# Kernel tuning notes

Hardware: AMD Instinct MI355X
Metric: run time of the kernel (lower is better)

Reference implementation:

```python
import jax, jax.numpy as jnp
import numpy as np

N1, N2, N3 = 262144, 65536, 16384
E1, E2 = 524288, 262144
IN_DIM, HID, HEADS, OUT_DIM = 128, 64, 4, 64
NEG_SLOPE = 0.2   # PyG GATConv default negative_slope
BN_EPS = 1e-5


def setup_inputs() -> dict:
    key = jax.random.key(0)
    ks = jax.random.split(key, 13)
    g = lambda k, shape, scale: jax.random.normal(k, shape, jnp.float32) * scale
    HD = HEADS * HID
    return {
        "x": jax.random.normal(ks[0], (N1, IN_DIM), jnp.float32),
        "W1_src": g(ks[1], (IN_DIM, HD), 1.0 / np.sqrt(IN_DIM)),
        "W1_dst": g(ks[2], (IN_DIM, HD), 1.0 / np.sqrt(IN_DIM)),
        "att1_src": g(ks[3], (HEADS, HID), 1.0 / np.sqrt(HID)),
        "att1_dst": g(ks[4], (HEADS, HID), 1.0 / np.sqrt(HID)),
        "b1": jnp.zeros((HD,), jnp.float32),
        "gamma": jnp.ones((HD,), jnp.float32),
        "beta": jnp.zeros((HD,), jnp.float32),
        "run_mean": jnp.zeros((HD,), jnp.float32),
        "run_var": jnp.ones((HD,), jnp.float32),
        "W2_src": g(ks[5], (HD, OUT_DIM), 1.0 / np.sqrt(HD)),
        "W2_dst": g(ks[6], (HD, OUT_DIM), 1.0 / np.sqrt(HD)),
        "att2_src": g(ks[7], (1, OUT_DIM), 1.0 / np.sqrt(OUT_DIM)),
        "att2_dst": g(ks[8], (1, OUT_DIM), 1.0 / np.sqrt(OUT_DIM)),
        "b2": jnp.zeros((OUT_DIM,), jnp.float32),
        "src1": jax.random.randint(ks[9], (E1,), 0, N1),
        "dst1": jax.random.randint(ks[10], (E1,), 0, N2),
        "src2": jax.random.randint(ks[11], (E2,), 0, N2),
        "dst2": jax.random.randint(ks[12], (E2,), 0, N3),
    }


def gat_conv(x_src, x_dst, W_src, W_dst, att_src, att_dst, bias, src, dst, num_dst, heads, ch):
    """PyG GATConv (bipartite, add_self_loops=False, concat)."""
    h_src = (x_src @ W_src).reshape(-1, heads, ch)   # [N, H, C]
    h_dst = (x_dst @ W_dst).reshape(-1, heads, ch)   # [M, H, C]
    a_src = jnp.sum(h_src * att_src, axis=-1)        # [N, H]
    a_dst = jnp.sum(h_dst * att_dst, axis=-1)        # [M, H]
    e = a_src[src] + a_dst[dst]                      # [E, H] gather
    e = jnp.where(e > 0, e, NEG_SLOPE * e)           # leaky_relu
    # segment softmax over destination nodes
    emax = jax.ops.segment_max(e, dst, num_segments=num_dst)
    emax = jax.lax.stop_gradient(jnp.where(jnp.isfinite(emax), emax, 0.0))
    p = jnp.exp(e - emax[dst])
    denom = jax.ops.segment_sum(p, dst, num_segments=num_dst)
    alpha = p / jnp.maximum(denom[dst], 1e-16)       # [E, H]
    msg = alpha[:, :, None] * h_src[src]             # [E, H, C]
    out = jax.ops.segment_sum(msg, dst, num_segments=num_dst)  # scatter-add
    return out.reshape(num_dst, heads * ch) + bias


def reference(x, W1_src, W1_dst, att1_src, att1_dst, b1, gamma, beta, run_mean, run_var,
              W2_src, W2_dst, att2_src, att2_dst, b2, src1, dst1, src2, dst2):
    # layer 1: GATConv((x, x_target), edge_index) with 4 heads, concat
    h = gat_conv(x, x[:N2], W1_src, W1_dst, att1_src, att1_dst, b1,
                 src1, dst1, N2, HEADS, HID)
    # BatchNorm1d in eval mode (running stats), then ELU; dropout is identity in eval
    h = (h - run_mean) * gamma / jnp.sqrt(run_var + BN_EPS) + beta
    h = jax.nn.elu(h)
    # layer 2: GATConv with heads=1
    out = gat_conv(h, h[:N3], W2_src, W2_dst, att2_src, att2_dst, b2,
                   src2, dst2, N3, 1, OUT_DIM)
    return out
```

## Files before the change

### kernel.cpp

```cpp
#include <hip/hip_runtime.h>


constexpr int N1 = 262144, N2 = 65536, N3 = 16384;
constexpr int E1 = 524288, E2 = 262144;
constexpr int IN_DIM = 128, HID = 64, HEADS = 4, OUT_DIM = 64;
constexpr int HD = HEADS * HID;
constexpr float NEG_SLOPE = 0.2f;
constexpr float BN_EPS = 1e-5f;

typedef __attribute__((ext_vector_type(8))) short bf16x8;
typedef __attribute__((ext_vector_type(8))) unsigned short ushort8;
typedef __attribute__((ext_vector_type(4))) float f32x4;

#define GLOAD_LDS16(gp, lp)                                              \
  __builtin_amdgcn_global_load_lds(                                      \
      (const __attribute__((address_space(1))) unsigned int*)(gp),       \
      (__attribute__((address_space(3))) unsigned int*)(lp), 16, 0, 0)

__device__ inline unsigned short f2bf(float f) {
  unsigned u = __float_as_uint(f);
  u += 0x7FFFu + ((u >> 16) & 1u);
  return (unsigned short)(u >> 16);
}

__global__ __launch_bounds__(256) void setup_k(
    const float* __restrict__ W1s, const float* __restrict__ W1d,
    const float* __restrict__ A1s, const float* __restrict__ A1d,
    const float* __restrict__ W2s, const float* __restrict__ W2d,
    const float* __restrict__ A2s, const float* __restrict__ A2d,
    const float* __restrict__ b1, const float* __restrict__ gamma,
    const float* __restrict__ beta, const float* __restrict__ mean,
    const float* __restrict__ var,
    float* __restrict__ wa1s, float* __restrict__ wa1d,
    float* __restrict__ wa2s, float* __restrict__ wa2d,
    float* __restrict__ bnsc, float* __restrict__ bnsh,
    int* __restrict__ deg1, int* __restrict__ deg2,
    int* __restrict__ rp1, int* __restrict__ rp2,
    float* __restrict__ a2s, float* __restrict__ a2d,
    unsigned short* __restrict__ w1T, unsigned short* __restrict__ w2T) {
  int b = blockIdx.x, tid = threadIdx.x;
  if (b < 4) {
    int t = b * 256 + tid;
    if (t < HEADS * IN_DIM) {
      int h = t >> 7, k = t & 127;
      float s = 0.f, d = 0.f;
      for (int c = 0; c < HID; ++c) {
        s += W1s[k * HD + h * HID + c] * A1s[h * HID + c];
        d += W1d[k * HD + h * HID + c] * A1d[h * HID + c];
      }
      wa1s[t] = s; wa1d[t] = d;
    } else if (t < HEADS * IN_DIM + HD) {
      int k = t - HEADS * IN_DIM;
      float s = 0.f, d = 0.f;
      for (int c = 0; c < OUT_DIM; ++c) {
        s += W2s[k * OUT_DIM + c] * A2s[c];
        d += W2d[k * OUT_DIM + c] * A2d[c];
      }
      wa2s[k] = s; wa2d[k] = d;
    } else if (t < HEADS * IN_DIM + 2 * HD) {
      int c = t - HEADS * IN_DIM - HD;
      float sc = gamma[c] * rsqrtf(var[c] + BN_EPS);
      bnsc[c] = sc;
      bnsh[c] = beta[c] + (b1[c] - mean[c]) * sc;
    }
  } else if (b < 68) {
    int i = (b - 4) * 256 + tid;
    int stride = 64 * 256;
    for (int j = i; j < N2; j += stride) { deg1[j] = 0; a2s[j] = 0.f; }
    for (int j = i; j < N3; j += stride) { deg2[j] = 0; a2d[j] = 0.f; }
    if (i == 0) { rp1[0] = 0; rp2[0] = 0; }
  } else if (b < 84) {
    int t = (b - 68) * 256 + tid;
    int n = t >> 4, g = t & 15;
    ushort8 o;
#pragma unroll
    for (int j = 0; j < 8; ++j) o[j] = f2bf(W1s[(size_t)(g * 8 + j) * HD + n]);
    *reinterpret_cast<ushort8*>(w1T + (size_t)n * IN_DIM + (size_t)(g ^ (n & 7)) * 8) = o;
  } else {
    int t = (b - 84) * 256 + tid;
    int n = t >> 5, G = t & 31;
    int k0 = G * 8;
    ushort8 o;
#pragma unroll
    for (int j = 0; j < 8; ++j) o[j] = f2bf(W2s[(size_t)(k0 + j) * OUT_DIM + n]);
    int idx = ((k0 >> 7) << 7) + ((k0 & 127) ^ ((n & 7) << 3));
    *reinterpret_cast<ushort8*>(w2T + (size_t)n * HD + idx) = o;
  }
}

__global__ __launch_bounds__(256) void hist12_k(
    const int* __restrict__ dst1, int* __restrict__ deg1, int* __restrict__ rank1,
    const int* __restrict__ dst2, int* __restrict__ deg2, int* __restrict__ rank2) {
  int b = blockIdx.x;
  if (b < E1 / 256) {
    int i = b * 256 + threadIdx.x;
    rank1[i] = atomicAdd(&deg1[dst1[i]], 1);
  } else {
    int i = (b - E1 / 256) * 256 + threadIdx.x;
    rank2[i] = atomicAdd(&deg2[dst2[i]], 1);
  }
}

__device__ inline void scan_body(const int* in, int* out, int* bsums, int n, int b) {
  __shared__ int s[256];
  int tid = threadIdx.x;
  int i0 = b * 1024 + tid * 4;
  int x0 = in[i0], x1 = in[i0 + 1], x2 = in[i0 + 2], x3 = in[i0 + 3];
  int t = x0 + x1 + x2 + x3;
  s[tid] = t;
  __syncthreads();
  for (int off = 1; off < 256; off <<= 1) {
    int v = (tid >= off) ? s[tid - off] : 0;
    __syncthreads();
    s[tid] += v;
    __syncthreads();
  }
  int base = s[tid] - t;
  out[i0] = base + x0;
  out[i0 + 1] = base + x0 + x1;
  out[i0 + 2] = base + x0 + x1 + x2;
  out[i0 + 3] = base + t;
  if (tid == 255) bsums[b] = s[255];
  (void)n;
}

__global__ __launch_bounds__(256) void scanA_k(
    const int* __restrict__ deg1, int* __restrict__ o1, int* __restrict__ bs1,
    const int* __restrict__ deg2, int* __restrict__ o2, int* __restrict__ bs2) {
  int b = blockIdx.x;
  if (b < 64) scan_body(deg1, o1, bs1, N2, b);
  else scan_body(deg2, o2, bs2, N3, b - 64);
}

__global__ void scanB_k(int* __restrict__ bs1, int* __restrict__ bs2) {
  __shared__ int s[256];
  int* bs = (blockIdx.x == 0) ? bs1 : bs2;
  int nb = (blockIdx.x == 0) ? 64 : 16;
  int tid = threadIdx.x;
  s[tid] = (tid < nb) ? bs[tid] : 0;
  __syncthreads();
  for (int off = 1; off < 256; off <<= 1) {
    int v = (tid >= off) ? s[tid - off] : 0;
    __syncthreads();
    s[tid] += v;
    __syncthreads();
  }
  if (tid < nb) bs[tid] = s[tid];
}

__global__ __launch_bounds__(256) void scanC_k(
    int* __restrict__ o1, const int* __restrict__ bs1,
    int* __restrict__ o2, const int* __restrict__ bs2) {
  int b = blockIdx.x;
  int* out; const int* bs; int bb;
  if (b < 64) { out = o1; bs = bs1; bb = b; }
  else { out = o2; bs = bs2; bb = b - 64; }
  if (bb == 0) return;
  int add = bs[bb - 1];
  int i0 = bb * 1024 + threadIdx.x * 4;
  out[i0] += add; out[i0 + 1] += add; out[i0 + 2] += add; out[i0 + 3] += add;
}

__global__ __launch_bounds__(256) void conv_scores1(
    const float* __restrict__ x, const float* __restrict__ wa_s,
    const float* __restrict__ wa_d, float* __restrict__ a_src,
    float* __restrict__ a_dst) {
  __shared__ float ws[HEADS * IN_DIM], wd[HEADS * IN_DIM];
  int tid = threadIdx.x;
  for (int i = tid; i < HEADS * IN_DIM; i += 256) { ws[i] = wa_s[i]; wd[i] = wa_d[i]; }
  __syncthreads();
  int row = blockIdx.x * 16 + (tid >> 4);
  int g = tid & 15;
  float4 v0 = *reinterpret_cast<const float4*>(x + (size_t)row * IN_DIM + g * 8);
  float4 v1 = *reinterpret_cast<const float4*>(x + (size_t)row * IN_DIM + g * 8 + 4);
  float xv[8] = {v0.x, v0.y, v0.z, v0.w, v1.x, v1.y, v1.z, v1.w};
#pragma unroll
  for (int h = 0; h < HEADS; ++h) {
    float p = 0.f;
#pragma unroll
    for (int j = 0; j < 8; ++j) p = fmaf(xv[j], ws[h * IN_DIM + g * 8 + j], p);
#pragma unroll
    for (int off = 1; off < 16; off <<= 1) p += __shfl_xor(p, off, 64);
    if (g == 0) a_src[(size_t)row * HEADS + h] = p;
  }
  if (row < N2) {
#pragma unroll
    for (int h = 0; h < HEADS; ++h) {
      float p = 0.f;
#pragma unroll
      for (int j = 0; j < 8; ++j) p = fmaf(xv[j], wd[h * IN_DIM + g * 8 + j], p);
#pragma unroll
      for (int off = 1; off < 16; off <<= 1) p += __shfl_xor(p, off, 64);
      if (g == 0) a_dst[(size_t)row * HEADS + h] = p;
    }
  }
}

__global__ __launch_bounds__(256) void scatter1p_k(
    const int* __restrict__ src, const int* __restrict__ dst,
    const int* __restrict__ rp, const int* __restrict__ rank,
    const float* __restrict__ a1s, const float* __restrict__ a1d,
    int* __restrict__ srcs, float4* __restrict__ pexp) {
  int i = blockIdx.x * 256 + threadIdx.x;
  int s = src[i], d = dst[i];
  float4 as = *reinterpret_cast<const float4*>(a1s + (size_t)s * HEADS);
  float4 ad = *reinterpret_cast<const float4*>(a1d + (size_t)d * HEADS);
  float4 p;
#pragma unroll
  for (int h = 0; h < 4; ++h) {
    float e = ((const float*)&as)[h] + ((const float*)&ad)[h];
    e = e > 0.f ? e : NEG_SLOPE * e;
    ((float*)&p)[h] = __expf(e);
  }
  int pos = rp[d] + rank[i];
  srcs[pos] = s;
  pexp[pos] = p;
}

__global__ __launch_bounds__(256) void agg1x(
    const int* __restrict__ rp, const int* __restrict__ srcs,
    const float4* __restrict__ pexp, const float* __restrict__ x,
    unsigned short* __restrict__ z) {
  int d = blockIdx.x * 4 + (threadIdx.x >> 6);
  int lane = threadIdx.x & 63;
  int beg = rp[d], end = rp[d + 1];
  float z0[4] = {0.f, 0.f, 0.f, 0.f}, z1[4] = {0.f, 0.f, 0.f, 0.f};
  float ss[4] = {0.f, 0.f, 0.f, 0.f}, ss2[4] = {0.f, 0.f, 0.f, 0.f};
  int j = beg;
  for (; j + 2 <= end; j += 2) {
    int s0 = srcs[j], s1 = srcs[j + 1];
    float4 p0 = pexp[j], p1 = pexp[j + 1];
    float2 v0 = *reinterpret_cast<const float2*>(x + (size_t)s0 * IN_DIM + lane * 2);
    float2 v1 = *reinterpret_cast<const float2*>(x + (size_t)s1 * IN_DIM + lane * 2);
#pragma unroll
    for (int h = 0; h < 4; ++h) {
      float ph0 = ((const float*)&p0)[h], ph1 = ((const float*)&p1)[h];
      z0[h] = fmaf(ph0, v0.x, fmaf(ph1, v1.x, z0[h]));
      z1[h] = fmaf(ph0, v0.y, fmaf(ph1, v1.y, z1[h]));
      ss[h] += ph0; ss2[h] += ph1;
    }
  }
  if (j < end) {
    int s0 = srcs[j];
    float4 p0 = pexp[j];
    float2 v0 = *reinterpret_cast<const float2*>(x + (size_t)s0 * IN_DIM + lane * 2);
#pragma unroll
    for (int h = 0; h < 4; ++h) {
      float ph0 = ((const float*)&p0)[h];
      z0[h] = fmaf(ph0, v0.x, z0[h]);
      z1[h] = fmaf(ph0, v0.y, z1[h]);
      ss[h] += ph0;
    }
  }
  int G = lane >> 2;
  int idx = ((G ^ (d & 7)) << 3) + ((lane & 3) << 1);
#pragma unroll
  for (int h = 0; h < 4; ++h) {
    float inv = 1.f / fmaxf(ss[h] + ss2[h], 1e-30f);
    unsigned out = (unsigned)f2bf(z0[h] * inv) | ((unsigned)f2bf(z1[h] * inv) << 16);
    *reinterpret_cast<unsigned*>(z + ((size_t)h * N2 + d) * IN_DIM + idx) = out;
  }
}

__global__ __launch_bounds__(256) void finalize1(
    const unsigned short* __restrict__ z, const unsigned short* __restrict__ w1T,
    const float* __restrict__ bnsc, const float* __restrict__ bnsh,
    const float* __restrict__ wa2s, const float* __restrict__ wa2d,
    unsigned short* __restrict__ acc1, float* __restrict__ a2s,
    float* __restrict__ a2d) {
  __shared__ char sm[49152];
  const int tid = threadIdx.x, wave = tid >> 6, lane = tid & 63;
  const int row0 = blockIdx.x * 128;
  const int h = blockIdx.y;
  const char* gA = (const char*)(z + ((size_t)h * N2 + row0) * IN_DIM);
  const char* gB = (const char*)(w1T + (size_t)h * 64 * IN_DIM);
#pragma unroll
  for (int it = 0; it < 8; ++it) {
    int off = it * 4096 + wave * 1024 + lane * 16;
    GLOAD_LDS16(gA + off, sm + off);
  }
#pragma unroll
  for (int it = 0; it < 4; ++it) {
    int off = it * 4096 + wave * 1024 + lane * 16;
    GLOAD_LDS16(gB + off, sm + 32768 + off);
  }
  __syncthreads();
  const int rbase = wave * 32;
  const int kl = (lane >> 4) * 8, fr = lane & 15;
  f32x4 acc[2][4] = {};
#pragma unroll
  for (int ks = 0; ks < 4; ++ks) {
    int k0 = ks * 32 + kl;
    bf16x8 a[2], b[4];
#pragma unroll
    for (int i = 0; i < 2; ++i) {
      int ra = rbase + i * 16 + fr;
      a[i] = *reinterpret_cast<const bf16x8*>(
          sm + ((size_t)ra * 128 + (k0 ^ ((ra & 7) << 3))) * 2);
    }
#pragma unroll
    for (int jj = 0; jj < 4; ++jj) {
      int cb = jj * 16 + fr;
      b[jj] = *reinterpret_cast<const bf16x8*>(
          sm + 32768 + ((size_t)cb * 128 + (k0 ^ ((cb & 7) << 3))) * 2);
    }
#pragma unroll
    for (int i = 0; i < 2; ++i)
#pragma unroll
      for (int jj = 0; jj < 4; ++jj)
        acc[i][jj] = __builtin_amdgcn_mfma_f32_16x16x32_bf16(a[i], b[jj], acc[i][jj], 0, 0, 0);
  }
  float sc[4], sh[4], w2sv[4], w2dv[4];
#pragma unroll
  for (int jj = 0; jj < 4; ++jj) {
    int c = h * 64 + jj * 16 + fr;
    sc[jj] = bnsc[c]; sh[jj] = bnsh[c]; w2sv[jj] = wa2s[c]; w2dv[jj] = wa2d[c];
  }
  const int g = lane >> 4;
#pragma unroll
  for (int i = 0; i < 2; ++i) {
#pragma unroll
    for (int q = 0; q < 4; ++q) {
      int row = row0 + rbase + i * 16 + g * 4 + q;
      float s2s = 0.f, s2d = 0.f;
#pragma unroll
      for (int jj = 0; jj < 4; ++jj) {
        float v = acc[i][jj][q] * sc[jj] + sh[jj];
        v = v > 0.f ? v : expm1f(v);
        s2s = fmaf(v, w2sv[jj], s2s);
        s2d = fmaf(v, w2dv[jj], s2d);
        int c = h * 64 + jj * 16 + fr;
        int idx = ((c >> 7) << 7) + ((c & 127) ^ ((row & 7) << 3));
        acc1[(size_t)row * HD + idx] = f2bf(v);
      }
#pragma unroll
      for (int off = 1; off < 16; off <<= 1) {
        s2s += __shfl_xor(s2s, off, 64);
        s2d += __shfl_xor(s2d, off, 64);
      }
      if (fr == 0) {
        atomicAdd(&a2s[row], s2s);
        if (row < N3) atomicAdd(&a2d[row], s2d);
      }
    }
  }
}

__global__ __launch_bounds__(256) void scatter2p_k(
    const int* __restrict__ src, const int* __restrict__ dst,
    const int* __restrict__ rp, const int* __restrict__ rank,
    const float* __restrict__ a2s, const float* __restrict__ a2d,
    int* __restrict__ srcs, float* __restrict__ pexp) {
  int i = blockIdx.x * 256 + threadIdx.x;
  int s = src[i], d = dst[i];
  float e = a2s[s] + a2d[d];
  e = e > 0.f ? e : NEG_SLOPE * e;
  int pos = rp[d] + rank[i];
  srcs[pos] = s;
  pexp[pos] = __expf(e);
}

__global__ __launch_bounds__(256) void gemm2(
    const unsigned short* __restrict__ acc1, const unsigned short* __restrict__ w2T,
    float* __restrict__ h2) {
  __shared__ char sm[65536];
  const int tid = threadIdx.x, wave = tid >> 6, lane = tid & 63;
  const int row0 = blockIdx.x * 128;
  const char* gB = (const char*)w2T;
#pragma unroll
  for (int it = 0; it < 8; ++it) {
    int off = it * 4096 + wave * 1024 + lane * 16;
    GLOAD_LDS16(gB + off, sm + 32768 + off);
  }
  const int rbase = wave * 32;
  const int kl = (lane >> 4) * 8, fr = lane & 15;
  f32x4 acc[2][4] = {};
  for (int kh = 0; kh < 2; ++kh) {
    __syncthreads();
#pragma unroll
    for (int it = 0; it < 8; ++it) {
      int r = it * 16 + (tid >> 4);
      const char* srcp = (const char*)(acc1 + (size_t)(row0 + r) * HD) +
                         kh * 256 + (tid & 15) * 16;
      GLOAD_LDS16(srcp, sm + it * 4096 + tid * 16);
    }
    __syncthreads();
#pragma unroll
    for (int ks = 0; ks < 4; ++ks) {
      int k0 = ks * 32 + kl;
      bf16x8 a[2], b[4];
#pragma unroll
      for (int i = 0; i < 2; ++i) {
        int ra = rbase + i * 16 + fr;
        a[i] = *reinterpret_cast<const bf16x8*>(
            sm + ((size_t)ra * 128 + (k0 ^ ((ra & 7) << 3))) * 2);
      }
#pragma unroll
      for (int jj = 0; jj < 4; ++jj) {
        int cb = jj * 16 + fr;
        b[jj] = *reinterpret_cast<const bf16x8*>(
            sm + 32768 + ((size_t)cb * 256 + kh * 128 + (k0 ^ ((cb & 7) << 3))) * 2);
      }
#pragma unroll
      for (int i = 0; i < 2; ++i)
#pragma unroll
        for (int jj = 0; jj < 4; ++jj)
          acc[i][jj] = __builtin_amdgcn_mfma_f32_16x16x32_bf16(a[i], b[jj], acc[i][jj], 0, 0, 0);
    }
  }
  const int g = lane >> 4;
#pragma unroll
  for (int i = 0; i < 2; ++i)
#pragma unroll
    for (int q = 0; q < 4; ++q) {
      int row = row0 + rbase + i * 16 + g * 4 + q;
#pragma unroll
      for (int jj = 0; jj < 4; ++jj)
        h2[(size_t)row * OUT_DIM + jj * 16 + fr] = acc[i][jj][q];
    }
}

__global__ __launch_bounds__(256) void agg2(
    const int* __restrict__ rp, const int* __restrict__ srcs,
    const float* __restrict__ pe, const float* __restrict__ h2,
    const float* __restrict__ b2, float* __restrict__ out) {
  int d = blockIdx.x * 4 + (threadIdx.x >> 6);
  int lane = threadIdx.x & 63;
  int beg = rp[d], end = rp[d + 1];
  float ssum = 0.f, ssum2 = 0.f, acc = 0.f, acc2 = 0.f;
  int j = beg;
  for (; j + 2 <= end; j += 2) {
    int s0 = srcs[j], s1 = srcs[j + 1];
    float p0 = pe[j], p1 = pe[j + 1];
    float v0 = h2[(size_t)s0 * OUT_DIM + lane];
    float v1 = h2[(size_t)s1 * OUT_DIM + lane];
    acc = fmaf(p0, v0, acc); acc2 = fmaf(p1, v1, acc2);
    ssum += p0; ssum2 += p1;
  }
  if (j < end) {
    int s0 = srcs[j];
    float p0 = pe[j];
    acc = fmaf(p0, h2[(size_t)s0 * OUT_DIM + lane], acc);
    ssum += p0;
  }
  acc += acc2; ssum += ssum2;
  out[(size_t)d * OUT_DIM + lane] = acc / fmaxf(ssum, 1e-30f) + b2[lane];
}

extern "C" void kernel_launch(void* const* d_in, const int* in_sizes, int n_in,
                              void* d_out, int out_size, void* d_ws, size_t ws_size,
                              hipStream_t stream) {
  const float* x     = (const float*)d_in[0];
  const float* W1s   = (const float*)d_in[1];
  const float* W1d   = (const float*)d_in[2];
  const float* A1s   = (const float*)d_in[3];
  const float* A1d   = (const float*)d_in[4];
  const float* b1    = (const float*)d_in[5];
  const float* gamma = (const float*)d_in[6];
  const float* beta  = (const float*)d_in[7];
  const float* rmean = (const float*)d_in[8];
  const float* rvar  = (const float*)d_in[9];
  const float* W2s   = (const float*)d_in[10];
  const float* W2d   = (const float*)d_in[11];
  const float* A2s   = (const float*)d_in[12];
  const float* A2d   = (const float*)d_in[13];
  const float* b2    = (const float*)d_in[14];
  const int* src1    = (const int*)d_in[15];
  const int* dst1    = (const int*)d_in[16];
  const int* src2    = (const int*)d_in[17];
  const int* dst2    = (const int*)d_in[18];
  (void)in_sizes; (void)n_in; (void)out_size; (void)ws_size;

  char* W = (char*)d_ws;
  size_t off = 0;
  auto alloc = [&](size_t bytes) { void* p = W + off; off = (off + bytes + 255) & ~(size_t)255; return p; };
  unsigned short* z    = (unsigned short*)alloc((size_t)HEADS * N2 * IN_DIM * 2);
  unsigned short* w1T  = (unsigned short*)alloc((size_t)HD * IN_DIM * 2);
  unsigned short* w2T  = (unsigned short*)alloc((size_t)OUT_DIM * HD * 2);
  unsigned short* acc1 = (unsigned short*)alloc((size_t)N2 * HD * 2);
  float* h2    = (float*)alloc((size_t)N2 * OUT_DIM * 4);
  float* a1s   = (float*)alloc((size_t)N1 * HEADS * 4);
  float* a1d   = (float*)alloc((size_t)N2 * HEADS * 4);
  float* a2s   = (float*)alloc((size_t)N2 * 4);
  float* a2d   = (float*)alloc((size_t)N3 * 4);
  float4* pexp1 = (float4*)alloc((size_t)E1 * 16);
  float* pexp2 = (float*)alloc((size_t)E2 * 4);
  int* deg1    = (int*)alloc((size_t)N2 * 4);
  int* rank1   = (int*)alloc((size_t)E1 * 4);
  int* rp1     = (int*)alloc((size_t)(N2 + 1) * 4);
  int* srcs1   = (int*)alloc((size_t)E1 * 4);
  int* deg2    = (int*)alloc((size_t)N3 * 4);
  int* rank2   = (int*)alloc((size_t)E2 * 4);
  int* rp2     = (int*)alloc((size_t)(N3 + 1) * 4);
  int* srcs2   = (int*)alloc((size_t)E2 * 4);
  float* wa1s  = (float*)alloc(HEADS * IN_DIM * 4);
  float* wa1d  = (float*)alloc(HEADS * IN_DIM * 4);
  float* wa2s  = (float*)alloc(HD * 4);
  float* wa2d  = (float*)alloc(HD * 4);
  float* bnsc  = (float*)alloc(HD * 4);
  float* bnsh  = (float*)alloc(HD * 4);
  int* bsums1  = (int*)alloc(64 * 4);
  int* bsums2  = (int*)alloc(64 * 4);

  setup_k<<<92, 256, 0, stream>>>(W1s, W1d, A1s, A1d, W2s, W2d, A2s, A2d,
                                  b1, gamma, beta, rmean, rvar,
                                  wa1s, wa1d, wa2s, wa2d, bnsc, bnsh,
                                  deg1, deg2, rp1, rp2, a2s, a2d, w1T, w2T);
  hist12_k<<<E1 / 256 + E2 / 256, 256, 0, stream>>>(dst1, deg1, rank1,
                                                    dst2, deg2, rank2);
  scanA_k<<<80, 256, 0, stream>>>(deg1, rp1 + 1, bsums1, deg2, rp2 + 1, bsums2);
  scanB_k<<<2, 256, 0, stream>>>(bsums1, bsums2);
  scanC_k<<<80, 256, 0, stream>>>(rp1 + 1, bsums1, rp2 + 1, bsums2);

  conv_scores1<<<N1 / 16, 256, 0, stream>>>(x, wa1s, wa1d, a1s, a1d);
  scatter1p_k<<<E1 / 256, 256, 0, stream>>>(src1, dst1, rp1, rank1, a1s, a1d,
                                            srcs1, pexp1);
  agg1x<<<N2 / 4, 256, 0, stream>>>(rp1, srcs1, pexp1, x, z);
  finalize1<<<dim3(N2 / 128, HEADS), 256, 0, stream>>>(
      z, w1T, bnsc, bnsh, wa2s, wa2d, acc1, a2s, a2d);

  scatter2p_k<<<E2 / 256, 256, 0, stream>>>(src2, dst2, rp2, rank2, a2s, a2d,
                                            srcs2, pexp2);
  gemm2<<<N2 / 128, 256, 0, stream>>>(acc1, w2T, h2);
  agg2<<<N3 / 4, 256, 0, stream>>>(rp2, srcs2, pexp2, h2, b2, (float*)d_out);
}
```

Before: 424.0 us.

## Gather bf16 copies of x and h2 in aggregations; fold scanB into scanC

After: 424.1 us. About the same (+0.0%).

```diff
diff --git a/kernel.cpp b/kernel.cpp
--- a/kernel.cpp
+++ b/kernel.cpp
@@ -22,6 +22,8 @@
   u += 0x7FFFu + ((u >> 16) & 1u);
   return (unsigned short)(u >> 16);
 }
+__device__ inline float bf2f_lo(unsigned v) { return __uint_as_float(v << 16); }
+__device__ inline float bf2f_hi(unsigned v) { return __uint_as_float(v & 0xffff0000u); }
 
 __global__ __launch_bounds__(256) void setup_k(
     const float* __restrict__ W1s, const float* __restrict__ W1d,
@@ -101,7 +103,7 @@
   }
 }
 
-__device__ inline void scan_body(const int* in, int* out, int* bsums, int n, int b) {
+__device__ inline void scan_body(const int* in, int* out, int* bsums, int b) {
   __shared__ int s[256];
   int tid = threadIdx.x;
   int i0 = b * 1024 + tid * 4;
@@ -121,50 +123,42 @@
   out[i0 + 2] = base + x0 + x1 + x2;
   out[i0 + 3] = base + t;
   if (tid == 255) bsums[b] = s[255];
-  (void)n;
 }
 
 __global__ __launch_bounds__(256) void scanA_k(
     const int* __restrict__ deg1, int* __restrict__ o1, int* __restrict__ bs1,
     const int* __restrict__ deg2, int* __restrict__ o2, int* __restrict__ bs2) {
   int b = blockIdx.x;
-  if (b < 64) scan_body(deg1, o1, bs1, N2, b);
-  else scan_body(deg2, o2, bs2, N3, b - 64);
-}
-
-__global__ void scanB_k(int* __restrict__ bs1, int* __restrict__ bs2) {
-  __shared__ int s[256];
-  int* bs = (blockIdx.x == 0) ? bs1 : bs2;
-  int nb = (blockIdx.x == 0) ? 64 : 16;
-  int tid = threadIdx.x;
-  s[tid] = (tid < nb) ? bs[tid] : 0;
-  __syncthreads();
-  for (int off = 1; off < 256; off <<= 1) {
-    int v = (tid >= off) ? s[tid - off] : 0;
-    __syncthreads();
-    s[tid] += v;
-    __syncthreads();
-  }
-  if (tid < nb) bs[tid] = s[tid];
+  if (b < 64) scan_body(deg1, o1, bs1, b);
+  else scan_body(deg2, o2, bs2, b - 64);
 }
 
 __global__ __launch_bounds__(256) void scanC_k(
     int* __restrict__ o1, const int* __restrict__ bs1,
     int* __restrict__ o2, const int* __restrict__ bs2) {
+  __shared__ int sadd;
   int b = blockIdx.x;
   int* out; const int* bs; int bb;
   if (b < 64) { out = o1; bs = bs1; bb = b; }
   else { out = o2; bs = bs2; bb = b - 64; }
+  int tid = threadIdx.x;
+  if (tid < 64) {
+    int v = (tid < bb) ? bs[tid] : 0;
+#pragma unroll
+    for (int off = 32; off; off >>= 1) v += __shfl_xor(v, off, 64);
+    if (tid == 0) sadd = v;
+  }
+  __syncthreads();
   if (bb == 0) return;
-  int add = bs[bb - 1];
-  int i0 = bb * 1024 + threadIdx.x * 4;
+  int add = sadd;
+  int i0 = bb * 1024 + tid * 4;
   out[i0] += add; out[i0 + 1] += add; out[i0 + 2] += add; out[i0 + 3] += add;
 }
 
 __global__ __launch_bounds__(256) void conv_scores1(
     const float* __restrict__ x, const float* __restrict__ wa_s,
-    const float* __restrict__ wa_d, float* __restrict__ a_src,
-    float* __restrict__ a_dst) {
+    const float* __restrict__ wa_d, unsigned short* __restrict__ xbf,
+    float* __restrict__ a_src, float* __restrict__ a_dst) {
   __shared__ float ws[HEADS * IN_DIM], wd[HEADS * IN_DIM];
   int tid = threadIdx.x;
   for (int i = tid; i < HEADS * IN_DIM; i += 256) { ws[i] = wa_s[i]; wd[i] = wa_d[i]; }
@@ -174,6 +168,10 @@
   float4 v0 = *reinterpret_cast<const float4*>(x + (size_t)row * IN_DIM + g * 8);
   float4 v1 = *reinterpret_cast<const float4*>(x + (size_t)row * IN_DIM + g * 8 + 4);
   float xv[8] = {v0.x, v0.y, v0.z, v0.w, v1.x, v1.y, v1.z, v1.w};
+  ushort8 o;
+#pragma unroll
+  for (int j = 0; j < 8; ++j) o[j] = f2bf(xv[j]);
+  *reinterpret_cast<ushort8*>(xbf + (size_t)row * IN_DIM + g * 8) = o;
 #pragma unroll
   for (int h = 0; h < HEADS; ++h) {
     float p = 0.f;
@@ -219,7 +217,7 @@
 
 __global__ __launch_bounds__(256) void agg1x(
     const int* __restrict__ rp, const int* __restrict__ srcs,
-    const float4* __restrict__ pexp, const float* __restrict__ x,
+    const float4* __restrict__ pexp, const unsigned short* __restrict__ xbf,
     unsigned short* __restrict__ z) {
   int d = blockIdx.x * 4 + (threadIdx.x >> 6);
   int lane = threadIdx.x & 63;
@@ -230,25 +228,28 @@
   for (; j + 2 <= end; j += 2) {
     int s0 = srcs[j], s1 = srcs[j + 1];
     float4 p0 = pexp[j], p1 = pexp[j + 1];
-    float2 v0 = *reinterpret_cast<const float2*>(x + (size_t)s0 * IN_DIM + lane * 2);
-    float2 v1 = *reinterpret_cast<const float2*>(x + (size_t)s1 * IN_DIM + lane * 2);
+    unsigned u0 = ((const unsigned*)(xbf + (size_t)s0 * IN_DIM))[lane];
+    unsigned u1 = ((const unsigned*)(xbf + (size_t)s1 * IN_DIM))[lane];
+    float v0x = bf2f_lo(u0), v0y = bf2f_hi(u0);
+    float v1x = bf2f_lo(u1), v1y = bf2f_hi(u1);
 #pragma unroll
     for (int h = 0; h < 4; ++h) {
       float ph0 = ((const float*)&p0)[h], ph1 = ((const float*)&p1)[h];
-      z0[h] = fmaf(ph0, v0.x, fmaf(ph1, v1.x, z0[h]));
-      z1[h] = fmaf(ph0, v0.y, fmaf(ph1, v1.y, z1[h]));
+      z0[h] = fmaf(ph0, v0x, fmaf(ph1, v1x, z0[h]));
+      z1[h] = fmaf(ph0, v0y, fmaf(ph1, v1y, z1[h]));
       ss[h] += ph0; ss2[h] += ph1;
     }
   }
   if (j < end) {
     int s0 = srcs[j];
     float4 p0 = pexp[j];
-    float2 v0 = *reinterpret_cast<const float2*>(x + (size_t)s0 * IN_DIM + lane * 2);
+    unsigned u0 = ((const unsigned*)(xbf + (size_t)s0 * IN_DIM))[lane];
+    float v0x = bf2f_lo(u0), v0y = bf2f_hi(u0);
 #pragma unroll
     for (int h = 0; h < 4; ++h) {
       float ph0 = ((const float*)&p0)[h];
-      z0[h] = fmaf(ph0, v0.x, z0[h]);
-      z1[h] = fmaf(ph0, v0.y, z1[h]);
+      z0[h] = fmaf(ph0, v0x, z0[h]);
+      z1[h] = fmaf(ph0, v0y, z1[h]);
       ss[h] += ph0;
     }
   }
@@ -362,7 +363,7 @@
 
 __global__ __launch_bounds__(256) void gemm2(
     const unsigned short* __restrict__ acc1, const unsigned short* __restrict__ w2T,
-    float* __restrict__ h2) {
+    unsigned short* __restrict__ h2bf) {
   __shared__ char sm[65536];
   const int tid = threadIdx.x, wave = tid >> 6, lane = tid & 63;
   const int row0 = blockIdx.x * 128;
@@ -416,13 +417,13 @@
       int row = row0 + rbase + i * 16 + g * 4 + q;
 #pragma unroll
       for (int jj = 0; jj < 4; ++jj)
-        h2[(size_t)row * OUT_DIM + jj * 16 + fr] = acc[i][jj][q];
+        h2bf[(size_t)row * OUT_DIM + jj * 16 + fr] = f2bf(acc[i][jj][q]);
     }
 }
 
 __global__ __launch_bounds__(256) void agg2(
     const int* __restrict__ rp, const int* __restrict__ srcs,
-    const float* __restrict__ pe, const float* __restrict__ h2,
+    const float* __restrict__ pe, const unsigned short* __restrict__ h2bf,
     const float* __restrict__ b2, float* __restrict__ out) {
   int d = blockIdx.x * 4 + (threadIdx.x >> 6);
   int lane = threadIdx.x & 63;
@@ -432,15 +433,16 @@
   for (; j + 2 <= end; j += 2) {
     int s0 = srcs[j], s1 = srcs[j + 1];
     float p0 = pe[j], p1 = pe[j + 1];
-    float v0 = h2[(size_t)s0 * OUT_DIM + lane];
-    float v1 = h2[(size_t)s1 * OUT_DIM + lane];
+    float v0 = __uint_as_float((unsigned)h2bf[(size_t)s0 * OUT_DIM + lane] << 16);
+    float v1 = __uint_as_float((unsigned)h2bf[(size_t)s1 * OUT_DIM + lane] << 16);
     acc = fmaf(p0, v0, acc); acc2 = fmaf(p1, v1, acc2);
     ssum += p0; ssum2 += p1;
   }
   if (j < end) {
     int s0 = srcs[j];
     float p0 = pe[j];
-    acc = fmaf(p0, h2[(size_t)s0 * OUT_DIM + lane], acc);
+    float v0 = __uint_as_float((unsigned)h2bf[(size_t)s0 * OUT_DIM + lane] << 16);
+    acc = fmaf(p0, v0, acc);
     ssum += p0;
   }
   acc += acc2; ssum += ssum2;
@@ -474,11 +476,12 @@
   char* W = (char*)d_ws;
   size_t off = 0;
   auto alloc = [&](size_t bytes) { void* p = W + off; off = (off + bytes + 255) & ~(size_t)255; return p; };
+  unsigned short* xbf  = (unsigned short*)alloc((size_t)N1 * IN_DIM * 2);
   unsigned short* z    = (unsigned short*)alloc((size_t)HEADS * N2 * IN_DIM * 2);
   unsigned short* w1T  = (unsigned short*)alloc((size_t)HD * IN_DIM * 2);
   unsigned short* w2T  = (unsigned short*)alloc((size_t)OUT_DIM * HD * 2);
   unsigned short* acc1 = (unsigned short*)alloc((size_t)N2 * HD * 2);
-  float* h2    = (float*)alloc((size_t)N2 * OUT_DIM * 4);
+  unsigned short* h2bf = (unsigned short*)alloc((size_t)N2 * OUT_DIM * 2);
   float* a1s   = (float*)alloc((size_t)N1 * HEADS * 4);
   float* a1d   = (float*)alloc((size_t)N2 * HEADS * 4);
   float* a2s   = (float*)alloc((size_t)N2 * 4);
@@ -509,18 +512,17 @@
   hist12_k<<<E1 / 256 + E2 / 256, 256, 0, stream>>>(dst1, deg1, rank1,
                                                     dst2, deg2, rank2);
   scanA_k<<<80, 256, 0, stream>>>(deg1, rp1 + 1, bsums1, deg2, rp2 + 1, bsums2);
-  scanB_k<<<2, 256, 0, stream>>>(bsums1, bsums2);
   scanC_k<<<80, 256, 0, stream>>>(rp1 + 1, bsums1, rp2 + 1, bsums2);
 
-  conv_scores1<<<N1 / 16, 256, 0, stream>>>(x, wa1s, wa1d, a1s, a1d);
+  conv_scores1<<<N1 / 16, 256, 0, stream>>>(x, wa1s, wa1d, xbf, a1s, a1d);
   scatter1p_k<<<E1 / 256, 256, 0, stream>>>(src1, dst1, rp1, rank1, a1s, a1d,
                                             srcs1, pexp1);
-  agg1x<<<N2 / 4, 256, 0, stream>>>(rp1, srcs1, pexp1, x, z);
+  agg1x<<<N2 / 4, 256, 0, stream>>>(rp1, srcs1, pexp1, xbf, z);
   finalize1<<<dim3(N2 / 128, HEADS), 256, 0, stream>>>(
       z, w1T, bnsc, bnsh, wa2s, wa2d, acc1, a2s, a2d);
 
   scatter2p_k<<<E2 / 256, 256, 0, stream>>>(src2, dst2, rp2, rank2, a2s, a2d,
                                             srcs2, pexp2);
-  gemm2<<<N2 / 128, 256, 0, stream>>>(acc1, w2T, h2);
-  agg2<<<N3 / 4, 256, 0, stream>>>(rp2, srcs2, pexp2, h2, b2, (float*)d_out);
-}
+  gemm2<<<N2 / 128, 256, 0, stream>>>(acc1, w2T, h2bf);
+  agg2<<<N3 / 4, 256, 0, stream>>>(rp2, srcs2, pexp2, h2bf, b2, (float*)d_out);
+}
```
